# Kernel optimization log

Measured on AMD Instinct MI355X. Metric: run time of the kernel, lower is better.

Reference implementation:

```python
import jax, jax.numpy as jnp
import numpy as np

B, IN_C, OUT_C, H, W = 16, 64, 64, 128, 128
MIN_R, MAX_R, BASE, SCALE = 1, 6, 3, 3


def setup_inputs() -> dict:
    key = jax.random.key(0)
    k1, k2 = jax.random.split(key)
    x = jax.random.normal(k1, (B, IN_C, H, W), dtype=jnp.float32)
    # kaiming-uniform-ish scale for a 3x3 conv weight
    weight = jax.random.normal(k2, (OUT_C, IN_C, 3, 3), dtype=jnp.float32) * (1.0 / np.sqrt(IN_C * 9))
    # truncated-normal-style integer dilation per output channel (deterministic)
    rng = np.random.default_rng(0)
    offsets = np.clip(np.round(rng.normal(BASE, SCALE, size=OUT_C)), MIN_R, MAX_R).astype(np.int32)
    return {"x": x, "weight": weight, "offsets": offsets}


def _gsd_conv(x, weight, offs_np):
    # Per-channel dilation conv: group channels by dilation, conv each group
    # (dilation=o, padding=o keeps HxW), scatter back to original channel order.
    out = jnp.zeros((x.shape[0], weight.shape[0], x.shape[2], x.shape[3]), dtype=x.dtype)
    for o in np.unique(offs_np):
        idx = np.nonzero(offs_np == o)[0]          # static channel indices for this dilation
        w = weight[idx]                             # [g, in_c, 3, 3]
        o = int(o)
        y = jax.lax.conv_general_dilated(
            x, w,
            window_strides=(1, 1),
            padding=[(o, o), (o, o)],
            rhs_dilation=(o, o),
            dimension_numbers=("NCHW", "OIHW", "NCHW"),
        )                                           # [B, g, H, W]
        out = out.at[:, idx].set(y)
    return out


def reference(x, weight, offsets):
    offs_np = np.asarray(offsets)
    return _gsd_conv(x, weight, offs_np)
```

## Files before the change

### kernel.cpp

```cpp
#include <hip/hip_runtime.h>


#define HW_ 128
#define C_ 64
#define B_ 16
#define EX 44
#define EY 28
#define NPIX (EY * EX)
#define NSETS 39
#define HALFDW (NPIX * 4)
#define PLANEDW (NSETS * 64 * 4)
#define PADW 140
#define PLANE_STRIDE (PADW * PADW * 16)
#define MAX_ITEMS 12
#define WS_WPACK_OFF 1024
#define WS_XB16_OFF (1 << 20)
#define XB16_BYTES ((size_t)B_ * 4 * PLANE_STRIDE * 2)


typedef __attribute__((ext_vector_type(8))) short short8;
typedef __attribute__((ext_vector_type(16))) float floatx16;

__device__ __forceinline__ unsigned bf16rne(float f) {
  unsigned u = __float_as_uint(f);
  return (u + 0x7FFFu + ((u >> 16) & 1u)) >> 16;
}

#define GLOAD_LDS16(g, l)                                   \
  __builtin_amdgcn_global_load_lds(                         \
      (const __attribute__((address_space(1))) void*)(g),   \
      (__attribute__((address_space(3))) void*)(l), 16, 0, 0)

__global__ __launch_bounds__(256) void gsd_prep(
    const float* __restrict__ x, const int* __restrict__ offsets,
    const float* __restrict__ w, int* __restrict__ desc,
    uint4* __restrict__ wpack, unsigned short* __restrict__ xb16,
    const int nrow) {
  const int bid = blockIdx.x;
  const int tid = threadIdx.x;

  if (bid < nrow) {
    const int b = bid / PADW, py = bid - b * PADW;
    uint4* o4 = (uint4*)xb16;
    const size_t pb0 = ((size_t)b * 4) * 39200 + (size_t)py * 280;
    const uint4 z = make_uint4(0, 0, 0, 0);
    if (py < 6 || py >= PADW - 6) {
      for (int i = tid; i < 1120; i += 256) {
        const int ks = i / 280, r = i - ks * 280;
        o4[pb0 + (size_t)ks * 39200 + r] = z;
      }
      return;
    }
    if (tid < 96) {
      const int ks = tid / 24, rr = tid - ks * 24;
      const int idx = rr < 12 ? rr : 256 + rr;
      o4[pb0 + (size_t)ks * 39200 + idx] = z;
    }
    const int y = py - 6;
    __shared__ unsigned l32[128 * 33];
    const int xx = tid & 127, ph = tid >> 7;
    const float* xp = x + (size_t)b * (C_ * HW_ * HW_) + y * HW_ + xx;
#pragma unroll 4
    for (int p = ph; p < 32; p += 2) {
      const float v0 = xp[(2 * p) * (HW_ * HW_)];
      const float v1 = xp[(2 * p + 1) * (HW_ * HW_)];
      l32[xx * 33 + p] = bf16rne(v0) | (bf16rne(v1) << 16);
    }
    __syncthreads();
#pragma unroll 4
    for (int ch = tid; ch < 1024; ch += 256) {
      const int ks = ch >> 8, r = ch & 255;
      const unsigned* s = &l32[(r >> 1) * 33 + ks * 8 + (r & 1) * 4];
      o4[pb0 + (size_t)ks * 39200 + 12 + r] = make_uint4(s[0], s[1], s[2], s[3]);
    }
    return;
  }

  __shared__ int sd[128];
  __shared__ int soffs[C_];
  if (tid < C_) soffs[tid] = offsets[tid];
  __syncthreads();
  if (tid < C_) {
    const int key = soffs[tid];
    int rank = 0;
    for (int c = 0; c < C_; ++c) {
      const int kc = soffs[c];
      rank += (int)((kc < key) | ((kc == key) & (c < tid)));
    }
    sd[rank] = tid;
  }
  __syncthreads();
  if (tid == 0) {
    int ni = 0, c = 0;
    while (c < C_ && ni < MAX_ITEMS) {
      const int d = soffs[sd[c]];
      int e = c;
      while (e < C_ && soffs[sd[e]] == d) ++e;
      for (int st = c; st < e && ni < MAX_ITEMS; st += 32) {
        sd[66 + ni] = d;
        sd[78 + ni] = st;
        sd[90 + ni] = (e - st) < 32 ? (e - st) : 32;
        ++ni;
      }
      c = e;
    }
    sd[64] = ni;
  }
  __syncthreads();

  const int sbid = bid - nrow;
  if (sbid == 0) {
    if (tid < 102) desc[tid] = sd[tid];
    return;
  }
  const int wix = sbid - 1;
  if (wix >= sd[64]) return;
  const int start = sd[78 + wix];
  const int g = sd[90 + wix];

  for (int i = tid; i < 4 * 9 * 64; i += 256) {
    const int ks = i / 576;
    const int r = i % 576;
    const int tap = r >> 6;
    const int lane = r & 63;
    const int m = lane & 31, hh = lane >> 5;
    const bool act = m < g;
    const int oc = act ? sd[start + m] : 0;
    unsigned ww[4];
    for (int jj = 0; jj < 4; ++jj) {
      float v0 = 0.f, v1 = 0.f;
      if (act) {
        const int ic0 = ks * 16 + hh * 8 + jj * 2;
        v0 = w[(oc * C_ + ic0) * 9 + tap];
        v1 = w[(oc * C_ + ic0 + 1) * 9 + tap];
      }
      ww[jj] = bf16rne(v0) | (bf16rne(v1) << 16);
    }
    wpack[(size_t)wix * 2304 + i] = make_uint4(ww[0], ww[1], ww[2], ww[3]);
  }
}

template <bool PRE>
__global__ __launch_bounds__(512, 2) void gsd_conv(
    const float* __restrict__ x, const unsigned short* __restrict__ xb16,
    const int* __restrict__ desc, const uint4* __restrict__ wpack,
    float* __restrict__ out) {
  const int tid = threadIdx.x;
  const int bid0 = blockIdx.x;
  const int gxid = (bid0 & 7) * 64 + (bid0 >> 3);
  const int b = gxid >> 5;
  const int yt = (gxid >> 2) & 7;
  const int xt = gxid & 3;
  const int y0 = yt * 16, x0 = xt * 32;

  const int lane = tid & 63;
  const int n = lane & 31;
  const int h = lane >> 5;
  const int wv = tid >> 6;
  const int yb = wv * 2;

  __shared__ __align__(16) unsigned ldsbuf[4 * PLANEDW];

  if constexpr (PRE) {
    const unsigned short* xbase = xb16 + (size_t)b * 4 * PLANE_STRIDE;
    int srcoff[5];
#pragma unroll
    for (int j = 0; j < 5; ++j) {
      int q = (wv + j * 8) * 64 + lane;
      if (q > 2 * NPIX - 1) q = 2 * NPIX - 1;
      const int p = q >= NPIX ? 1 : 0;
      const int pix = q - p * NPIX;
      const int yy = pix / EX, xx = pix - yy * EX;
      srcoff[j] = ((y0 + yy) * PADW + (x0 + xx)) * 16 + p * 8;
    }
#pragma unroll
    for (int ks = 0; ks < 4; ++ks) {
      const unsigned short* xp = xbase + (size_t)ks * PLANE_STRIDE;
#pragma unroll
      for (int j = 0; j < 5; ++j) {
        if (j < 4 || wv < 7) {
          GLOAD_LDS16(xp + srcoff[j],
                      &ldsbuf[ks * PLANEDW + (wv + j * 8) * 256]);
        }
      }
    }
  } else {
    const int slx = tid & 63;
    const int sq = (tid >> 6) & 3;
    const int sy2 = tid >> 8;
    const float* xb = x + (size_t)b * (C_ * HW_ * HW_);
    const int gx = x0 - 6 + slx;
    const int gxc = gx < 0 ? 0 : (gx > 127 ? 127 : gx);
    const bool xin = ((unsigned)gx < 128u) & (slx < EX);
    for (int ks = 0; ks < 4; ++ks) {
      const float* xp = xb + (size_t)(ks * 16 + sq * 4) * (HW_ * HW_);
#pragma unroll 2
      for (int yy = sy2; yy < EY; yy += 2) {
        const int gy = y0 - 6 + yy;
        const int gyc = gy < 0 ? 0 : (gy > 127 ? 127 : gy);
        const bool ok = xin & ((unsigned)gy < 128u);
        const float* p = xp + gyc * HW_ + gxc;
        float v0 = p[0];
        float v1 = p[HW_ * HW_];
        float v2 = p[2 * HW_ * HW_];
        float v3 = p[3 * HW_ * HW_];
        if (!ok) { v0 = v1 = v2 = v3 = 0.f; }
        const unsigned lo = bf16rne(v0) | (bf16rne(v1) << 16);
        const unsigned hi = bf16rne(v2) | (bf16rne(v3) << 16);
        if (slx < EX) {
          const int pix = yy * EX + slx;
          const int dws = ks * PLANEDW + (sq >> 1) * HALFDW + pix * 4 +
                          ((sq & 1) << 1);
          *reinterpret_cast<uint2*>(&ldsbuf[dws]) = make_uint2(lo, hi);
        }
      }
    }
  }
  __syncthreads();

  const int cnt = __builtin_amdgcn_readfirstlane(desc[64]);
  const int hbase = h * HALFDW;

  for (int s = 0; s < cnt; ++s) {
    const int d = __builtin_amdgcn_readfirstlane(desc[66 + s]);
    const int start = __builtin_amdgcn_readfirstlane(desc[78 + s]);
    const int g = __builtin_amdgcn_readfirstlane(desc[90 + s]);

    const uint4* wp = wpack + (size_t)s * 2304 + lane;
    uint4 af[36];
#pragma unroll
    for (int i = 0; i < 36; ++i) af[i] = wp[i * 64];

    floatx16 acc0, acc1;
#pragma unroll
    for (int e = 0; e < 16; ++e) { acc0[e] = 0.f; acc1[e] = 0.f; }

#pragma unroll
    for (int i = 0; i < 36; ++i) {
      const int ks = i / 9, tap = i % 9;
      const int ky = tap / 3 - 1, kx = tap % 3 - 1;
      const int prow = yb + ky * d + 6;
      const int pxb = n + kx * d + 6;
      const int pix0 = prow * EX + pxb;
      const int pix1 = pix0 + EX;
      const unsigned* cb = &ldsbuf[ks * PLANEDW + hbase];
      const short8 bf0 = *reinterpret_cast<const short8*>(&cb[pix0 * 4]);
      const short8 bf1 = *reinterpret_cast<const short8*>(&cb[pix1 * 4]);
      const short8 a8 = __builtin_bit_cast(short8, af[i]);
      acc0 = __builtin_amdgcn_mfma_f32_32x32x16_bf16(a8, bf0, acc0, 0, 0, 0);
      acc1 = __builtin_amdgcn_mfma_f32_32x32x16_bf16(a8, bf1, acc1, 0, 0, 0);
    }

#pragma unroll
    for (int reg = 0; reg < 16; ++reg) {
      const int row = (reg & 3) + 8 * (reg >> 2) + 4 * h;
      if (row < g) {
        const int oc = desc[start + row];
        float* op =
            &out[((size_t)(b * C_ + oc) * HW_ + (y0 + yb)) * HW_ + x0 + n];
        op[0] = acc0[reg];
        op[HW_] = acc1[reg];
      }
    }
  }
}

extern "C" void kernel_launch(void* const* d_in, const int* in_sizes, int n_in,
                              void* d_out, int out_size, void* d_ws,
                              size_t ws_size, hipStream_t stream) {
  const float* x = (const float*)d_in[0];
  const float* w = (const float*)d_in[1];
  const int* offsets = (const int*)d_in[2];
  float* out = (float*)d_out;

  int* desc = (int*)d_ws;
  uint4* wpack = (uint4*)((char*)d_ws + WS_WPACK_OFF);
  unsigned short* xb16 = (unsigned short*)((char*)d_ws + WS_XB16_OFF);

  const bool pre = ws_size >= (size_t)WS_XB16_OFF + XB16_BYTES;
  const int nrow = pre ? B_ * PADW : 0;

  gsd_prep<<<dim3(nrow + 1 + MAX_ITEMS), 256, 0, stream>>>(
      x, offsets, w, desc, wpack, xb16, nrow);
  if (pre) {
    gsd_conv<true><<<dim3(B_ * 8 * 4), 512, 0, stream>>>(
        x, xb16, desc, wpack, out);
  } else {
    gsd_conv<false><<<dim3(B_ * 8 * 4), 512, 0, stream>>>(
        x, xb16, desc, wpack, out);
  }
}
```

Before: 211.3 us.

## Give each wave four output rows per dilation item and use 12-wave blocks

```diff
diff --git a/kernel.cpp b/kernel.cpp
--- a/kernel.cpp
+++ b/kernel.cpp
@@ -7,9 +7,12 @@
 #define EX 44
 #define EY 28
 #define NPIX (EY * EX)
-#define NSETS 39
-#define HALFDW (NPIX * 4)
-#define PLANEDW (NSETS * 64 * 4)
+#define CHPP (NPIX * 2)
+#define NCHTOT (CHPP * 4)
+#define NROUND 13
+#define LDSDW (NROUND * 768 * 4)
+#define PLDW (CHPP * 4)
+#define HDW (NPIX * 4)
 #define PADW 140
 #define PLANE_STRIDE (PADW * PADW * 16)
 #define MAX_ITEMS 12
@@ -141,7 +144,7 @@
 }
 
 template <bool PRE>
-__global__ __launch_bounds__(512, 2) void gsd_conv(
+__global__ __launch_bounds__(768, 3) void gsd_conv(
     const float* __restrict__ x, const unsigned short* __restrict__ xb16,
     const int* __restrict__ desc, const uint4* __restrict__ wpack,
     float* __restrict__ out) {
@@ -157,45 +160,40 @@
   const int n = lane & 31;
   const int h = lane >> 5;
   const int wv = tid >> 6;
-  const int yb = wv * 2;
-
-  __shared__ __align__(16) unsigned ldsbuf[4 * PLANEDW];
+
+  __shared__ __align__(16) unsigned ldsbuf[LDSDW];
 
   if constexpr (PRE) {
     const unsigned short* xbase = xb16 + (size_t)b * 4 * PLANE_STRIDE;
-    int srcoff[5];
-#pragma unroll
-    for (int j = 0; j < 5; ++j) {
-      int q = (wv + j * 8) * 64 + lane;
-      if (q > 2 * NPIX - 1) q = 2 * NPIX - 1;
-      const int p = q >= NPIX ? 1 : 0;
-      const int pix = q - p * NPIX;
+    int srcoff[NROUND];
+#pragma unroll
+    for (int r = 0; r < NROUND; ++r) {
+      int q = r * 768 + tid;
+      if (q > NCHTOT - 1) q = NCHTOT - 1;
+      const int plane = q / CHPP;
+      const int c = q - plane * CHPP;
+      const int p = c >= NPIX ? 1 : 0;
+      const int pix = c - p * NPIX;
       const int yy = pix / EX, xx = pix - yy * EX;
-      srcoff[j] = ((y0 + yy) * PADW + (x0 + xx)) * 16 + p * 8;
-    }
-#pragma unroll
-    for (int ks = 0; ks < 4; ++ks) {
-      const unsigned short* xp = xbase + (size_t)ks * PLANE_STRIDE;
-#pragma unroll
-      for (int j = 0; j < 5; ++j) {
-        if (j < 4 || wv < 7) {
-          GLOAD_LDS16(xp + srcoff[j],
-                      &ldsbuf[ks * PLANEDW + (wv + j * 8) * 256]);
-        }
-      }
+      srcoff[r] = plane * PLANE_STRIDE +
+                  ((y0 + yy) * PADW + (x0 + xx)) * 16 + p * 8;
+    }
+#pragma unroll
+    for (int r = 0; r < NROUND; ++r) {
+      GLOAD_LDS16(xbase + srcoff[r], &ldsbuf[(r * 768 + wv * 64) * 4]);
     }
   } else {
     const int slx = tid & 63;
-    const int sq = (tid >> 6) & 3;
-    const int sy2 = tid >> 8;
+    const int grp = tid >> 6;
+    const int sq = grp & 3;
+    const int sy3 = grp >> 2;
     const float* xb = x + (size_t)b * (C_ * HW_ * HW_);
     const int gx = x0 - 6 + slx;
     const int gxc = gx < 0 ? 0 : (gx > 127 ? 127 : gx);
     const bool xin = ((unsigned)gx < 128u) & (slx < EX);
     for (int ks = 0; ks < 4; ++ks) {
       const float* xp = xb + (size_t)(ks * 16 + sq * 4) * (HW_ * HW_);
-#pragma unroll 2
-      for (int yy = sy2; yy < EY; yy += 2) {
+      for (int yy = sy3; yy < EY; yy += 3) {
         const int gy = y0 - 6 + yy;
         const int gyc = gy < 0 ? 0 : (gy > 127 ? 127 : gy);
         const bool ok = xin & ((unsigned)gy < 128u);
@@ -209,8 +207,8 @@
         const unsigned hi = bf16rne(v2) | (bf16rne(v3) << 16);
         if (slx < EX) {
           const int pix = yy * EX + slx;
-          const int dws = ks * PLANEDW + (sq >> 1) * HALFDW + pix * 4 +
-                          ((sq & 1) << 1);
+          const int dws =
+              ks * PLDW + (sq >> 1) * HDW + pix * 4 + ((sq & 1) << 1);
           *reinterpret_cast<uint2*>(&ldsbuf[dws]) = make_uint2(lo, hi);
         }
       }
@@ -219,36 +217,44 @@
   __syncthreads();
 
   const int cnt = __builtin_amdgcn_readfirstlane(desc[64]);
-  const int hbase = h * HALFDW;
-
-  for (int s = 0; s < cnt; ++s) {
-    const int d = __builtin_amdgcn_readfirstlane(desc[66 + s]);
-    const int start = __builtin_amdgcn_readfirstlane(desc[78 + s]);
-    const int g = __builtin_amdgcn_readfirstlane(desc[90 + s]);
-
-    const uint4* wp = wpack + (size_t)s * 2304 + lane;
-    uint4 af[36];
-#pragma unroll
-    for (int i = 0; i < 36; ++i) af[i] = wp[i * 64];
-
-    floatx16 acc0, acc1;
-#pragma unroll
-    for (int e = 0; e < 16; ++e) { acc0[e] = 0.f; acc1[e] = 0.f; }
-
-#pragma unroll
-    for (int i = 0; i < 36; ++i) {
-      const int ks = i / 9, tap = i % 9;
-      const int ky = tap / 3 - 1, kx = tap % 3 - 1;
-      const int prow = yb + ky * d + 6;
-      const int pxb = n + kx * d + 6;
-      const int pix0 = prow * EX + pxb;
-      const int pix1 = pix0 + EX;
-      const unsigned* cb = &ldsbuf[ks * PLANEDW + hbase];
-      const short8 bf0 = *reinterpret_cast<const short8*>(&cb[pix0 * 4]);
-      const short8 bf1 = *reinterpret_cast<const short8*>(&cb[pix1 * 4]);
-      const short8 a8 = __builtin_bit_cast(short8, af[i]);
-      acc0 = __builtin_amdgcn_mfma_f32_32x32x16_bf16(a8, bf0, acc0, 0, 0, 0);
-      acc1 = __builtin_amdgcn_mfma_f32_32x32x16_bf16(a8, bf1, acc1, 0, 0, 0);
+
+  for (int s = wv; s < 4 * cnt; s += 12) {
+    const int quad = s / cnt;
+    const int item = s - quad * cnt;
+    const int d = __builtin_amdgcn_readfirstlane(desc[66 + item]);
+    const int start = __builtin_amdgcn_readfirstlane(desc[78 + item]);
+    const int g = __builtin_amdgcn_readfirstlane(desc[90 + item]);
+    const int yq = quad * 4;
+
+    floatx16 acc[4];
+#pragma unroll
+    for (int r = 0; r < 4; ++r)
+#pragma unroll
+      for (int e = 0; e < 16; ++e) acc[r][e] = 0.f;
+
+#pragma unroll
+    for (int ks = 0; ks < 4; ++ks) {
+      const uint4* wp = wpack + ((size_t)item * 4 + ks) * 576 + lane;
+      uint4 af[9];
+#pragma unroll
+      for (int t = 0; t < 9; ++t) af[t] = wp[t * 64];
+      const unsigned* cb = &ldsbuf[ks * PLDW + h * HDW];
+#pragma unroll
+      for (int tap = 0; tap < 9; ++tap) {
+        const int ky = tap / 3 - 1, kx = tap % 3 - 1;
+        const int prow = yq + ky * d + 6;
+        const int pxb = n + kx * d + 6;
+        const int pixb = prow * EX + pxb;
+        short8 bf[4];
+#pragma unroll
+        for (int r = 0; r < 4; ++r)
+          bf[r] = *reinterpret_cast<const short8*>(&cb[(pixb + r * EX) * 4]);
+        const short8 a8 = __builtin_bit_cast(short8, af[tap]);
+#pragma unroll
+        for (int r = 0; r < 4; ++r)
+          acc[r] =
+              __builtin_amdgcn_mfma_f32_32x32x16_bf16(a8, bf[r], acc[r], 0, 0, 0);
+      }
     }
 
 #pragma unroll
@@ -257,9 +263,9 @@
       if (row < g) {
         const int oc = desc[start + row];
         float* op =
-            &out[((size_t)(b * C_ + oc) * HW_ + (y0 + yb)) * HW_ + x0 + n];
-        op[0] = acc0[reg];
-        op[HW_] = acc1[reg];
+            &out[((size_t)(b * C_ + oc) * HW_ + (y0 + yq)) * HW_ + x0 + n];
+#pragma unroll
+        for (int r = 0; r < 4; ++r) op[r * HW_] = acc[r][reg];
       }
     }
   }
@@ -283,10 +289,10 @@
   gsd_prep<<<dim3(nrow + 1 + MAX_ITEMS), 256, 0, stream>>>(
       x, offsets, w, desc, wpack, xb16, nrow);
   if (pre) {
-    gsd_conv<true><<<dim3(B_ * 8 * 4), 512, 0, stream>>>(
+    gsd_conv<true><<<dim3(B_ * 8 * 4), 768, 0, stream>>>(
         x, xb16, desc, wpack, out);
   } else {
-    gsd_conv<false><<<dim3(B_ * 8 * 4), 512, 0, stream>>>(
+    gsd_conv<false><<<dim3(B_ * 8 * 4), 768, 0, stream>>>(
         x, xb16, desc, wpack, out);
   }
 }
```

New measurement: 200.4 us. 5.2% less time.
